# Kernel tuning notes

Measured on AMD Instinct MI355X. Metric: run time of the kernel, lower is better.

Reference implementation:

```python
import jax, jax.numpy as jnp
import numpy as np

L, E, N, D, A = 3, 1000000, 100000, 64, 8
NREL = 230
NR2 = 2 * NREL + 1  # 461 relation embeddings
Q, ENT = 1000, 10000


def setup_inputs() -> dict:
    key = jax.random.key(0)
    ks = jax.random.split(key, 21)
    p = lambda k, shape: jax.random.normal(k, shape, dtype=jnp.float32) * 0.1
    return {
        "relation": jax.random.randint(ks[0], (Q,), 0, NR2, dtype=jnp.int32),
        "r_idx": jax.random.randint(ks[1], (L, E), 0, Q, dtype=jnp.int32),
        "rel": jax.random.randint(ks[2], (L, E), 0, NR2, dtype=jnp.int32),
        "sub": jax.random.randint(ks[3], (L, E), 0, N, dtype=jnp.int32),
        "obj": jax.random.randint(ks[4], (L, E), 0, N, dtype=jnp.int32),
        "idx": jnp.arange(N, dtype=jnp.int32),
        "nodes_q": jax.random.randint(ks[5], (N,), 0, Q, dtype=jnp.int32),
        "nodes_ent": jax.random.randint(ks[6], (N,), 0, ENT, dtype=jnp.int32),
        "rela_embed": p(ks[7], (L, NR2, D)),
        "Ws_w": p(ks[8], (L, A, D)),
        "Wr_w": p(ks[9], (L, A, D)),
        "Wqr_w": p(ks[10], (L, A, D)),
        "Wqr_b": p(ks[11], (L, A)),
        "walpha_w": p(ks[12], (L, 1, A)),
        "walpha_b": p(ks[13], (L, 1)),
        "Wh_w": p(ks[14], (L, D, D)),
        "gru_Wih": p(ks[15], (3 * D, D)),
        "gru_Whh": p(ks[16], (3 * D, D)),
        "gru_bih": p(ks[17], (3 * D,)),
        "gru_bhh": p(ks[18], (3 * D,)),
        "Wfinal_w": p(ks[19], (1, D)),
    }


def _gru_cell(x, h, Wih, Whh, bih, bhh):
    # torch nn.GRU single step: gates from input x and state h
    gi = x @ Wih.T + bih  # [N, 3D]
    gh = h @ Whh.T + bhh  # [N, 3D]
    i_r, i_z, i_n = jnp.split(gi, 3, axis=-1)
    h_r, h_z, h_n = jnp.split(gh, 3, axis=-1)
    r = jax.nn.sigmoid(i_r + h_r)
    z = jax.nn.sigmoid(i_z + h_z)
    n = jnp.tanh(i_n + r * h_n)
    return (1.0 - z) * n + z * h


def reference(relation, r_idx, rel, sub, obj, idx, nodes_q, nodes_ent,
              rela_embed, Ws_w, Wr_w, Wqr_w, Wqr_b, walpha_w, walpha_b, Wh_w,
              gru_Wih, gru_Whh, gru_bih, gru_bhh, Wfinal_w):
    hidden = jnp.zeros((N, D), dtype=jnp.float32)
    h0 = jnp.zeros((N, D), dtype=jnp.float32)
    for i in range(L):  # small fixed number of structurally distinct layers
        emb = rela_embed[i]
        hs = hidden[sub[i]]              # [E, D] gather of source node states
        hr = emb[rel[i]]                 # [E, D] relation embedding lookup
        h_qr = emb[relation[r_idx[i]]]   # [E, D] query-relation embedding
        attn = jax.nn.relu(hs @ Ws_w[i].T + hr @ Wr_w[i].T + h_qr @ Wqr_w[i].T + Wqr_b[i])
        alpha = jax.nn.sigmoid(attn @ walpha_w[i].T + walpha_b[i])  # [E, 1]
        message = alpha * (hs + hr)
        agg = jax.ops.segment_sum(message, obj[i], num_segments=N)  # scatter-add
        hidden = jax.nn.relu(agg @ Wh_w[i].T)
        # index_copy of previous state into new node ordering
        h0 = jnp.zeros((N, D), dtype=jnp.float32).at[idx].set(h0)
        h0 = _gru_cell(hidden, h0, gru_Wih, gru_Whh, gru_bih, gru_bhh)
        hidden = h0
    scores = (hidden @ Wfinal_w.T)[:, 0]  # [N]
    scores_all = jnp.zeros((Q, ENT), dtype=jnp.float32).at[nodes_q, nodes_ent].set(scores)
    return scores_all
```

## Files before the change

### kernel.cpp

```cpp
#include <hip/hip_runtime.h>
#include <math.h>

#define LL  3
#define EE  1000000
#define NNODE 100000
#define DD  64
#define AAT 8
#define NR2C 461
#define QQ  1000
#define ENTC 10000
#define QE  (QQ * ENTC)

#define NB    782
#define NWGL  128
#define CHUNK 7813
#define CAPB  4096

#define SCAN_N (NB * NWGL)
#define SCAN_TILE 4096
#define SCAN_TILES ((SCAN_N + SCAN_TILE - 1) / SCAN_TILE)

#define NTILES (NNODE / 16)
#define NWTILES 58
#define FRAG_U4_PER_LAYER (NWTILES * 2 * 64)

typedef __attribute__((ext_vector_type(8))) short s8v;
typedef __attribute__((ext_vector_type(4))) float f4v;

__device__ __forceinline__ float sigmoidf_(float x) {
    return 1.0f / (1.0f + __expf(-x));
}
__device__ __forceinline__ float tanhf_(float x) {
    return 1.0f - 2.0f / (__expf(2.0f * x) + 1.0f);
}
__device__ __forceinline__ unsigned short bf16rne(float f) {
    unsigned u = __float_as_uint(f);
    return (unsigned short)((u + 0x7FFFu + ((u >> 16) & 1u)) >> 16);
}
__device__ __forceinline__ float bf16tof(unsigned short b) {
    return __uint_as_float(((unsigned)b) << 16);
}

__device__ __forceinline__ float dot8_reduce(float* p, int lane) {
#pragma unroll
    for (int st = 1; st < 8; st <<= 1)
#pragma unroll
        for (int a = 0; a < 8; ++a)
            p[a] += __shfl_xor(p[a], st, 64);
    const int aid = lane & 7;
    float v = p[0];
#pragma unroll
    for (int j = 1; j < 8; ++j)
        v = (aid == j) ? p[j] : v;
    v += __shfl_xor(v, 8, 64);
    v += __shfl_xor(v, 16, 64);
    v += __shfl_xor(v, 32, 64);
    return v;
}

__global__ void fill_f32(float* __restrict__ p, int n, float v) {
    int i = blockIdx.x * blockDim.x + threadIdx.x;
    int stride = gridDim.x * blockDim.x;
    float4* p4 = (float4*)p;
    int n4 = n >> 2;
    float4 v4 = make_float4(v, v, v, v);
    for (int j = i; j < n4; j += stride) p4[j] = v4;
}

__global__ void fill_i32(int* __restrict__ p, int n, int v) {
    int i = blockIdx.x * blockDim.x + threadIdx.x;
    int stride = gridDim.x * blockDim.x;
    int4* p4 = (int4*)p;
    int n4 = n >> 2;
    int4 v4 = make_int4(v, v, v, v);
    for (int j = i; j < n4; j += stride) p4[j] = v4;
}


__global__ __launch_bounds__(256) void part_hist(
    const int* __restrict__ obj, int* __restrict__ hist)
{
    const int l = blockIdx.y, wg = blockIdx.x;
    const int* o = obj + l * EE;
    __shared__ int cnt[NB];
    for (int b = threadIdx.x; b < NB; b += 256) cnt[b] = 0;
    __syncthreads();
    const int s = wg * CHUNK;
    const int e = (s + CHUNK < EE) ? s + CHUNK : EE;
    for (int p = s + threadIdx.x; p < e; p += 256)
        atomicAdd(&cnt[o[p] >> 7], 1);
    __syncthreads();
    int* hh = hist + l * (NB * NWGL);
    for (int b = threadIdx.x; b < NB; b += 256)
        hh[b * NWGL + wg] = cnt[b];
}

__global__ __launch_bounds__(1024) void scan_tiles_reduce(
    const int* __restrict__ hist, int* __restrict__ totals)
{
    const int l = blockIdx.y, tile = blockIdx.x;
    const int* hh = hist + l * SCAN_N;
    const int idx = tile * SCAN_TILE + threadIdx.x * 4;
    int s = 0;
    if (idx < SCAN_N) {
        const int4 v = *(const int4*)(hh + idx);
        s = v.x + v.y + v.z + v.w;
    }
#pragma unroll
    for (int st = 1; st < 64; st <<= 1) s += __shfl_xor(s, st, 64);
    __shared__ int ws[16];
    if ((threadIdx.x & 63) == 0) ws[threadIdx.x >> 6] = s;
    __syncthreads();
    if (threadIdx.x == 0) {
        int t = 0;
#pragma unroll
        for (int i = 0; i < 16; ++i) t += ws[i];
        totals[l * SCAN_TILES + tile] = t;
    }
}

__global__ __launch_bounds__(1024) void scan_tiles_scan(
    int* __restrict__ hist, const int* __restrict__ totals,
    int* __restrict__ bucketptr)
{
    const int l = blockIdx.y, tile = blockIdx.x;
    int* hh = hist + l * SCAN_N;
    int* bp = bucketptr + l * (NB + 1);
    const int t = threadIdx.x;
    __shared__ int lds[1024];
    __shared__ int toff_s;
    if (t < 64) {
        int o = (t < tile) ? totals[l * SCAN_TILES + t] : 0;
#pragma unroll
        for (int st = 1; st < 64; st <<= 1) o += __shfl_xor(o, st, 64);
        if (t == 0) toff_s = o;
    }
    const int idx = tile * SCAN_TILE + t * 4;
    int4 v = make_int4(0, 0, 0, 0);
    if (idx < SCAN_N) v = *(const int4*)(hh + idx);
    const int tsum = v.x + v.y + v.z + v.w;
    lds[t] = tsum;
    __syncthreads();
    for (int st = 1; st < 1024; st <<= 1) {
        const int u = (t >= st) ? lds[t - st] : 0;
        __syncthreads();
        lds[t] += u;
        __syncthreads();
    }
    const int excl = lds[t] - tsum + toff_s;
    if (idx < SCAN_N) {
        int4 o;
        o.x = excl;
        o.y = excl + v.x;
        o.z = o.y + v.y;
        o.w = o.z + v.z;
        *(int4*)(hh + idx) = o;
        if ((idx & 127) == 0) bp[idx >> 7] = o.x;
    }
    if (t == 0 && tile == 0) bp[NB] = EE;
}

__global__ __launch_bounds__(256) void part_scatter(
    const int* __restrict__ obj, const int* __restrict__ sub,
    const int* __restrict__ rel, const int* __restrict__ r_idx,
    const int* __restrict__ hist, unsigned long long* __restrict__ pk64)
{
    const int l = blockIdx.y, wg = blockIdx.x;
    const int* o  = obj + l * EE;
    const int* ss = sub + l * EE;
    const int* rr = rel + l * EE;
    const int* qq = r_idx + l * EE;
    unsigned long long* pk = pk64 + (size_t)l * EE;
    const int* hh = hist + l * (NB * NWGL);
    __shared__ int off[NB];
    for (int b = threadIdx.x; b < NB; b += 256) off[b] = hh[b * NWGL + wg];
    __syncthreads();
    const int s0 = wg * CHUNK;
    const int e0 = (s0 + CHUNK < EE) ? s0 + CHUNK : EE;
    for (int p = s0 + threadIdx.x; p < e0; p += 256) {
        const int ov = o[p];
        const int pos = atomicAdd(&off[ov >> 7], 1);
        pk[pos] = (unsigned long long)(unsigned)ss[p]
                | ((unsigned long long)(unsigned)rr[p] << 17)
                | ((unsigned long long)(unsigned)qq[p] << 26)
                | ((unsigned long long)(unsigned)(ov & 127) << 36);
    }
}

__global__ __launch_bounds__(256) void bucket_sort(
    const int* __restrict__ bucketptr, unsigned long long* __restrict__ pk64,
    int* __restrict__ rowptr)
{
    const int l = blockIdx.y, b = blockIdx.x;
    unsigned long long* pk = pk64 + (size_t)l * EE;
    const int* bp = bucketptr + l * (NB + 1);
    const int base = bp[b], endp = bp[b + 1];
    const int ne = endp - base;
    extern __shared__ unsigned long long stg[];
    __shared__ int cnt[128];
    __shared__ int off[128];
    const int t = threadIdx.x;
    if (t < 128) cnt[t] = 0;
    __syncthreads();
    for (int i = t; i < ne; i += 256) {
        const unsigned long long u = pk[base + i];
        stg[i] = u;
        atomicAdd(&cnt[(int)((u >> 36) & 127)], 1);
    }
    __syncthreads();
    if (t == 0) {
        int run = 0;
#pragma unroll 8
        for (int o2 = 0; o2 < 128; ++o2) { off[o2] = run; run += cnt[o2]; }
    }
    __syncthreads();
    if (t < 128) {
        const int node = b * 128 + t;
        if (node < NNODE) rowptr[l * NNODE + node] = base + off[t] + cnt[t];
    }
    __syncthreads();
    for (int i = t; i < ne; i += 256) {
        const unsigned long long u = stg[i];
        const int pos = base + atomicAdd(&off[(int)((u >> 36) & 127)], 1);
        pk[pos] = u;
    }
}


__global__ __launch_bounds__(256) void rqatt_kernel(
    const int* __restrict__ relation, const float* __restrict__ emb,
    const float* __restrict__ Wr, const float* __restrict__ Wqr,
    const float* __restrict__ Wqrb,
    float* __restrict__ r_att, float* __restrict__ qr_att)
{
    const int lane = threadIdx.x & 63;
    const int wid = (blockIdx.x * blockDim.x + threadIdx.x) >> 6;
    const int nw = (gridDim.x * blockDim.x) >> 6;
    float wr8[8], wq8[8];
#pragma unroll
    for (int a = 0; a < 8; ++a) {
        wr8[a] = Wr[a * 64 + lane];
        wq8[a] = Wqr[a * 64 + lane];
    }
    for (int i = wid; i < NR2C + QQ; i += nw) {
        const bool isQ = i >= NR2C;
        const int row = isQ ? relation[i - NR2C] : i;
        const float ev = emb[row * 64 + lane];
        float p[8];
#pragma unroll
        for (int a = 0; a < 8; ++a) p[a] = ev * (isQ ? wq8[a] : wr8[a]);
        float v = dot8_reduce(p, lane);
        if (lane < 8) {
            if (isQ) qr_att[(i - NR2C) * 8 + lane] = v + Wqrb[lane];
            else     r_att[i * 8 + lane] = v;
        }
    }
}

template<bool L0>
__global__ __launch_bounds__(256) void alpha_csr(
    const unsigned long long* __restrict__ pk64,
    const float* __restrict__ s_att, const float* __restrict__ r_att,
    const float* __restrict__ qr_att,
    const float* __restrict__ walw, const float* __restrict__ walb,
    float* __restrict__ alpha_p)
{
    const int e = blockIdx.x * blockDim.x + threadIdx.x;
    if (e >= EE) return;
    const unsigned long long u = pk64[e];
    const int s = (int)(u & 0x1FFFF);
    const int r = (int)((u >> 17) & 0x1FF);
    const int q = (int)((u >> 26) & 0x3FF);
    const float4* ra = (const float4*)(r_att + r * 8);
    const float4* qa = (const float4*)(qr_att + q * 8);
    const float4 r0 = ra[0], r1 = ra[1];
    const float4 q0 = qa[0], q1 = qa[1];
    float v0 = r0.x + q0.x, v1 = r0.y + q0.y, v2 = r0.z + q0.z, v3 = r0.w + q0.w;
    float v4 = r1.x + q1.x, v5 = r1.y + q1.y, v6 = r1.z + q1.z, v7 = r1.w + q1.w;
    if (!L0) {
        const float4* sa = (const float4*)(s_att + s * 8);
        const float4 s0 = sa[0], s1 = sa[1];
        v0 += s0.x; v1 += s0.y; v2 += s0.z; v3 += s0.w;
        v4 += s1.x; v5 += s1.y; v6 += s1.z; v7 += s1.w;
    }
    float t = walb[0];
    t += walw[0] * fmaxf(v0, 0.0f);
    t += walw[1] * fmaxf(v1, 0.0f);
    t += walw[2] * fmaxf(v2, 0.0f);
    t += walw[3] * fmaxf(v3, 0.0f);
    t += walw[4] * fmaxf(v4, 0.0f);
    t += walw[5] * fmaxf(v5, 0.0f);
    t += walw[6] * fmaxf(v6, 0.0f);
    t += walw[7] * fmaxf(v7, 0.0f);
    alpha_p[e] = sigmoidf_(t);
}

template<bool L0>
__device__ __forceinline__ float gather_term(
    const unsigned long long* __restrict__ pk64,
    const float* __restrict__ alpha_p, int p,
    const float* __restrict__ h, const float* __restrict__ emb, int lane)
{
    const unsigned long long u = pk64[p];
    const float a = alpha_p[p];
    const int s = (int)(u & 0x1FFFF);
    const int r = (int)((u >> 17) & 0x1FF);
    float m = emb[r * 64 + lane];
    if (!L0) m += h[s * 64 + lane];
    return a * m;
}

template<bool L0>
__global__ __launch_bounds__(256) void agg_gather(
    const int* __restrict__ rowptr, const unsigned long long* __restrict__ pk64,
    const float* __restrict__ alpha_p,
    const float* __restrict__ h, const float* __restrict__ emb,
    float* __restrict__ agg)
{
    const int lane = threadIdx.x & 63;
    const int wid = (blockIdx.x * blockDim.x + threadIdx.x) >> 6;
    const int nw = (gridDim.x * blockDim.x) >> 6;
    for (int n = wid; n < NNODE; n += nw) {
        const int start = __builtin_amdgcn_readfirstlane((n == 0) ? 0 : rowptr[n - 1]);
        const int end   = __builtin_amdgcn_readfirstlane(rowptr[n]);
        float a0 = 0.0f, a1 = 0.0f, a2 = 0.0f, a3 = 0.0f;
        int p = start;
        for (; p + 3 < end; p += 4) {
            a0 += gather_term<L0>(pk64, alpha_p, p,     h, emb, lane);
            a1 += gather_term<L0>(pk64, alpha_p, p + 1, h, emb, lane);
            a2 += gather_term<L0>(pk64, alpha_p, p + 2, h, emb, lane);
            a3 += gather_term<L0>(pk64, alpha_p, p + 3, h, emb, lane);
        }
        for (; p < end; ++p)
            a0 += gather_term<L0>(pk64, alpha_p, p, h, emb, lane);
        agg[n * 64 + lane] = (a0 + a1) + (a2 + a3);
    }
}


__global__ __launch_bounds__(128) void build_frags(
    const float* __restrict__ Wh_all, const float* __restrict__ Wih,
    const float* __restrict__ Whh, const float* __restrict__ Ws_all,
    uint4* __restrict__ frag)
{
    const int li = blockIdx.y;
    const int tile = blockIdx.x;
    const int term = threadIdx.x >> 6;
    const int lane_s = threadIdx.x & 63;
    const int rs = lane_s & 15, gs = lane_s >> 4;
    const float* Wh = Wh_all + li * DD * DD;
    const float* WsNext = Ws_all + (li + 1) * AAT * DD;
    unsigned short pk[8];
#pragma unroll
    for (int i = 0; i < 8; ++i) {
        const int kl = 16 * (i >> 2) + 4 * gs + (i & 3);
        float f;
        if (tile < 8)       { const int mt = tile >> 1, kf = tile & 1;
                              f = Wh[(mt * 16 + rs) * 64 + kf * 32 + kl]; }
        else if (tile < 40) { const int t2 = tile - 8, mt = t2 >> 2, kf = t2 & 3;
                              const int j = mt * 16 + rs, k = kf * 32 + kl;
                              f = (k < 64) ? Wih[j * 64 + k] : Whh[j * 64 + k - 64]; }
        else if (tile < 48) { const int t2 = tile - 40, mt = t2 >> 1, kf = t2 & 1;
                              f = Wih[(128 + mt * 16 + rs) * 64 + kf * 32 + kl]; }
        else if (tile < 56) { const int t2 = tile - 48, mt = t2 >> 1, kf = t2 & 1;
                              f = Whh[(128 + mt * 16 + rs) * 64 + kf * 32 + kl]; }
        else                { const int kf = tile - 56;
                              f = (li < 2 && rs < 8) ? WsNext[rs * 64 + kf * 32 + kl] : 0.0f; }
        if (term == 0) pk[i] = bf16rne(f);
        else { const float hi = bf16tof(bf16rne(f)); pk[i] = bf16rne(f - hi); }
    }
    uint4 w;
    w.x = (unsigned)pk[0] | ((unsigned)pk[1] << 16);
    w.y = (unsigned)pk[2] | ((unsigned)pk[3] << 16);
    w.z = (unsigned)pk[4] | ((unsigned)pk[5] << 16);
    w.w = (unsigned)pk[6] | ((unsigned)pk[7] << 16);
    frag[((size_t)li * NWTILES + tile) * 128 + term * 64 + lane_s] = w;
}

__device__ __forceinline__ void make_bfrag(const float* d16, s8v* hi, s8v* lo) {
#pragma unroll
    for (int t = 0; t < 2; ++t) {
        s8v hv, lv;
#pragma unroll
        for (int i = 0; i < 8; ++i) {
            const float f = d16[(2 * t + (i >> 2)) * 4 + (i & 3)];
            const unsigned short hb = bf16rne(f);
            hv[i] = (short)hb;
            lv[i] = (short)bf16rne(f - bf16tof(hb));
        }
        hi[t] = hv; lo[t] = lv;
    }
}

__device__ __forceinline__ f4v mm3(const s8v* __restrict__ afr, int tile, int lane,
                                   s8v bh, s8v bl, f4v c) {
    const s8v ah = afr[(tile * 2 + 0) * 64 + lane];
    const s8v al = afr[(tile * 2 + 1) * 64 + lane];
    c = __builtin_amdgcn_mfma_f32_16x16x32_bf16(ah, bh, c, 0, 0, 0);
    c = __builtin_amdgcn_mfma_f32_16x16x32_bf16(ah, bl, c, 0, 0, 0);
    c = __builtin_amdgcn_mfma_f32_16x16x32_bf16(al, bh, c, 0, 0, 0);
    return c;
}

__device__ __forceinline__ void ld16(const float* p, float* d) {
#pragma unroll
    for (int mt = 0; mt < 4; ++mt) {
        const float4 v = *(const float4*)(p + 16 * mt);
        d[mt * 4 + 0] = v.x; d[mt * 4 + 1] = v.y;
        d[mt * 4 + 2] = v.z; d[mt * 4 + 3] = v.w;
    }
}

template<bool L0, bool SATT, bool SCORE>
__global__ __launch_bounds__(256, 4) void node_mfma(
    const uint4* __restrict__ frag,
    const float* __restrict__ bih, const float* __restrict__ bhh,
    const float* __restrict__ Wf,
    float* __restrict__ h, const float* __restrict__ agg,
    float* __restrict__ s_att, float* __restrict__ scores)
{
    const int tid = threadIdx.x;
    const int lane = tid & 63;
    const int wslot = (blockIdx.x * 256 + tid) >> 6;
    const int base = wslot * 16;
    if (base >= NNODE) return;
    const int r = lane & 15, g = lane >> 4;
    const s8v* afr = (const s8v*)frag;

    float ag[16], hp[16];
    ld16(agg + (base + r) * 64 + 4 * g, ag);
    if (!L0) ld16(h + (base + r) * 64 + 4 * g, hp);
    else {
#pragma unroll
        for (int i = 0; i < 16; ++i) hp[i] = 0.0f;
    }
    s8v agh[2], agl[2];
    make_bfrag(ag, agh, agl);
    s8v hh2[2], hl2[2];
    if (!L0) make_bfrag(hp, hh2, hl2);

    float xd[16];
#pragma unroll
    for (int mt = 0; mt < 4; ++mt) {
        f4v acc = {0.0f, 0.0f, 0.0f, 0.0f};
        acc = mm3(afr, mt * 2 + 0, lane, agh[0], agl[0], acc);
        acc = mm3(afr, mt * 2 + 1, lane, agh[1], agl[1], acc);
#pragma unroll
        for (int c = 0; c < 4; ++c) xd[mt * 4 + c] = fmaxf(acc[c], 0.0f);
    }
    s8v xh[2], xl[2];
    make_bfrag(xd, xh, xl);

    f4v rz[8];
#pragma unroll
    for (int mt = 0; mt < 4; ++mt) {
        const int j0 = 16 * mt + 4 * g;
        const float4 a = *(const float4*)(bih + j0);
        const float4 b = *(const float4*)(bhh + j0);
        f4v t; t[0] = a.x + b.x; t[1] = a.y + b.y; t[2] = a.z + b.z; t[3] = a.w + b.w;
        rz[mt] = t;
        const float4 a2 = *(const float4*)(bih + 64 + j0);
        const float4 b2 = *(const float4*)(bhh + 64 + j0);
        f4v t2; t2[0] = a2.x + b2.x; t2[1] = a2.y + b2.y; t2[2] = a2.z + b2.z; t2[3] = a2.w + b2.w;
        rz[mt + 4] = t2;
    }
#pragma unroll
    for (int mt = 0; mt < 8; ++mt) {
        f4v acc = rz[mt];
        acc = mm3(afr, 8 + mt * 4 + 0, lane, xh[0], xl[0], acc);
        acc = mm3(afr, 8 + mt * 4 + 1, lane, xh[1], xl[1], acc);
        if (!L0) {
            acc = mm3(afr, 8 + mt * 4 + 2, lane, hh2[0], hl2[0], acc);
            acc = mm3(afr, 8 + mt * 4 + 3, lane, hh2[1], hl2[1], acc);
        }
        rz[mt] = acc;
    }

    f4v in4[4], hn4[4];
#pragma unroll
    for (int mt = 0; mt < 4; ++mt) {
        const int j0 = 16 * mt + 4 * g;
        const float4 a = *(const float4*)(bih + 128 + j0);
        f4v t; t[0] = a.x; t[1] = a.y; t[2] = a.z; t[3] = a.w;
        in4[mt] = t;
        const float4 b = *(const float4*)(bhh + 128 + j0);
        f4v t2; t2[0] = b.x; t2[1] = b.y; t2[2] = b.z; t2[3] = b.w;
        hn4[mt] = t2;
    }
#pragma unroll
    for (int mt = 0; mt < 4; ++mt) {
        f4v acc = in4[mt];
        acc = mm3(afr, 40 + mt * 2 + 0, lane, xh[0], xl[0], acc);
        acc = mm3(afr, 40 + mt * 2 + 1, lane, xh[1], xl[1], acc);
        in4[mt] = acc;
        if (!L0) {
            f4v a2 = hn4[mt];
            a2 = mm3(afr, 48 + mt * 2 + 0, lane, hh2[0], hl2[0], a2);
            a2 = mm3(afr, 48 + mt * 2 + 1, lane, hh2[1], hl2[1], a2);
            hn4[mt] = a2;
        }
    }

    float ho[16];
#pragma unroll
    for (int mt = 0; mt < 4; ++mt)
#pragma unroll
        for (int c = 0; c < 4; ++c) {
            const float rr = sigmoidf_(rz[mt][c]);
            const float zz = sigmoidf_(rz[mt + 4][c]);
            const float nn = tanhf_(in4[mt][c] + rr * hn4[mt][c]);
            ho[mt * 4 + c] = (1.0f - zz) * nn + zz * hp[mt * 4 + c];
        }

    if (!SCORE) {
        float* hop = h + (base + r) * 64 + 4 * g;
#pragma unroll
        for (int mt = 0; mt < 4; ++mt)
            *(float4*)(hop + 16 * mt) = make_float4(ho[mt * 4 + 0], ho[mt * 4 + 1],
                                                    ho[mt * 4 + 2], ho[mt * 4 + 3]);
    }
    if (SATT) {
        s8v oh[2], ol[2];
        make_bfrag(ho, oh, ol);
        f4v sa = {0.0f, 0.0f, 0.0f, 0.0f};
        sa = mm3(afr, 56, lane, oh[0], ol[0], sa);
        sa = mm3(afr, 57, lane, oh[1], ol[1], sa);
        if (g < 2) {
#pragma unroll
            for (int c = 0; c < 4; ++c)
                s_att[(base + r) * 8 + 4 * g + c] = sa[c];
        }
    }
    if (SCORE) {
        float s = 0.0f;
        const float* wfp = Wf + 4 * g;
#pragma unroll
        for (int mt = 0; mt < 4; ++mt) {
            const float4 w = *(const float4*)(wfp + 16 * mt);
            s += ho[mt * 4 + 0] * w.x + ho[mt * 4 + 1] * w.y
               + ho[mt * 4 + 2] * w.z + ho[mt * 4 + 3] * w.w;
        }
        s += __shfl_xor(s, 16, 64);
        s += __shfl_xor(s, 32, 64);
        if (lane < 16) scores[base + r] = s;
    }
}

__global__ void scatter_max_kernel(const int* __restrict__ nq, const int* __restrict__ ne,
                                   int* __restrict__ winner)
{
    int n = blockIdx.x * blockDim.x + threadIdx.x;
    if (n < NNODE) {
        int pos = nq[n] * ENTC + ne[n];
        atomicMax(&winner[pos], n);
    }
}

__global__ void scatter_write_kernel(const int* __restrict__ nq, const int* __restrict__ ne,
                                     const int* __restrict__ winner,
                                     const float* __restrict__ scores,
                                     float* __restrict__ out)
{
    int n = blockIdx.x * blockDim.x + threadIdx.x;
    if (n < NNODE) {
        int pos = nq[n] * ENTC + ne[n];
        if (winner[pos] == n) out[pos] = scores[n];
    }
}

extern "C" void kernel_launch(void* const* d_in, const int* in_sizes, int n_in,
                              void* d_out, int out_size, void* d_ws, size_t ws_size,
                              hipStream_t stream)
{
    const int* relation  = (const int*)d_in[0];
    const int* r_idx     = (const int*)d_in[1];
    const int* rel       = (const int*)d_in[2];
    const int* sub       = (const int*)d_in[3];
    const int* obj       = (const int*)d_in[4];
    const int* nodes_q   = (const int*)d_in[6];
    const int* nodes_ent = (const int*)d_in[7];
    const float* rela    = (const float*)d_in[8];
    const float* Ws      = (const float*)d_in[9];
    const float* Wr      = (const float*)d_in[10];
    const float* Wqr     = (const float*)d_in[11];
    const float* Wqrb    = (const float*)d_in[12];
    const float* walw    = (const float*)d_in[13];
    const float* walb    = (const float*)d_in[14];
    const float* Wh      = (const float*)d_in[15];
    const float* gWih    = (const float*)d_in[16];
    const float* gWhh    = (const float*)d_in[17];
    const float* gbih    = (const float*)d_in[18];
    const float* gbhh    = (const float*)d_in[19];
    const float* Wf      = (const float*)d_in[20];

    float* ws     = (float*)d_ws;
    float* scores = ws;
    float* h      = ws + 102400;
    float* agg    = h + NNODE * DD;
    int*   winner = (int*)(ws + 102400);
    float* out    = (float*)d_out;

    unsigned long long* pk64 = (unsigned long long*)d_out;
    uint4* fragbuf  = (uint4*)((float*)d_out + 6000000);
    float* s_att    = (float*)d_out + 6000000 + 3 * FRAG_U4_PER_LAYER * 4;
    float* r_att    = s_att + NNODE * 8;
    float* qr_att   = r_att + NR2C * 8;
    int*   rowptr   = (int*)(qr_att + QQ * 8);
    int*   hist     = rowptr + 3 * NNODE;
    int*   bucketpt = hist + 3 * NB * NWGL;
    int*   totals   = bucketpt + 3 * (NB + 1);
    float* alpha_p  = (float*)(totals + 3 * SCAN_TILES);

    part_hist<<<dim3(NWGL, 3), 256, 0, stream>>>(obj, hist);
    scan_tiles_reduce<<<dim3(SCAN_TILES, 3), 1024, 0, stream>>>(hist, totals);
    scan_tiles_scan<<<dim3(SCAN_TILES, 3), 1024, 0, stream>>>(hist, totals, bucketpt);
    part_scatter<<<dim3(NWGL, 3), 256, 0, stream>>>(obj, sub, rel, r_idx, hist, pk64);
    bucket_sort<<<dim3(NB, 3), 256, CAPB * 8, stream>>>(bucketpt, pk64, rowptr);
    build_frags<<<dim3(NWTILES, 3), 128, 0, stream>>>(Wh, gWih, gWhh, Ws, fragbuf);

    const int NODE_GRID = (NTILES * 64 + 255) / 256;
    for (int i = 0; i < LL; ++i) {
        const float* emb = rela + i * NR2C * DD;
        const uint4* fr = fragbuf + (size_t)i * FRAG_U4_PER_LAYER;
        rqatt_kernel<<<184, 256, 0, stream>>>(relation, emb,
            Wr + i * AAT * DD, Wqr + i * AAT * DD, Wqrb + i * AAT, r_att, qr_att);
        if (i == 0) {
            alpha_csr<true><<<(EE + 255) / 256, 256, 0, stream>>>(
                pk64, s_att, r_att, qr_att, walw, walb, alpha_p);
            agg_gather<true><<<2048, 256, 0, stream>>>(
                rowptr, pk64, alpha_p, h, emb, agg);
            node_mfma<true, true, false><<<NODE_GRID, 256, 0, stream>>>(
                fr, gbih, gbhh, Wf, h, agg, s_att, scores);
        } else {
            alpha_csr<false><<<(EE + 255) / 256, 256, 0, stream>>>(
                pk64 + (size_t)i * EE, s_att, r_att, qr_att,
                walw + i * AAT, walb + i, alpha_p);
            agg_gather<false><<<2048, 256, 0, stream>>>(
                rowptr + i * NNODE, pk64 + (size_t)i * EE, alpha_p, h, emb, agg);
            if (i == 1)
                node_mfma<false, true, false><<<NODE_GRID, 256, 0, stream>>>(
                    fr, gbih, gbhh, Wf, h, agg, s_att, scores);
            else
                node_mfma<false, false, true><<<NODE_GRID, 256, 0, stream>>>(
                    fr, gbih, gbhh, Wf, h, agg, s_att, scores);
        }
    }

    fill_f32<<<2048, 256, 0, stream>>>(out, QE, 0.0f);
    fill_i32<<<2048, 256, 0, stream>>>(winner, QE, -1);
    scatter_max_kernel<<<(NNODE + 255) / 256, 256, 0, stream>>>(nodes_q, nodes_ent, winner);
    scatter_write_kernel<<<(NNODE + 255) / 256, 256, 0, stream>>>(nodes_q, nodes_ent, winner, scores, out);
}
```

Measured before the change: 601.8 us.

## Stage partition scatter and bucket sort in LDS for coalesced global writes

```diff
diff --git a/kernel.cpp b/kernel.cpp
--- a/kernel.cpp
+++ b/kernel.cpp
@@ -16,6 +16,8 @@
 #define CHUNK 7813
 #define CAPB  4096
 
+#define PS_LDS (CHUNK * 8 + NB * 4 * 2 + 256 * 4)
+
 #define SCAN_N (NB * NWGL)
 #define SCAN_TILE 4096
 #define SCAN_TILES ((SCAN_N + SCAN_TILE - 1) / SCAN_TILE)
@@ -165,6 +167,10 @@
     const int* __restrict__ rel, const int* __restrict__ r_idx,
     const int* __restrict__ hist, unsigned long long* __restrict__ pk64)
 {
+    extern __shared__ unsigned long long stg[];
+    int* cnt   = (int*)(stg + CHUNK);
+    int* delta = cnt + NB;
+    int* psum  = delta + NB;
     const int l = blockIdx.y, wg = blockIdx.x;
     const int* o  = obj + l * EE;
     const int* ss = sub + l * EE;
@@ -172,18 +178,64 @@
     const int* qq = r_idx + l * EE;
     unsigned long long* pk = pk64 + (size_t)l * EE;
     const int* hh = hist + l * (NB * NWGL);
-    __shared__ int off[NB];
-    for (int b = threadIdx.x; b < NB; b += 256) off[b] = hh[b * NWGL + wg];
-    __syncthreads();
+    const int t = threadIdx.x;
     const int s0 = wg * CHUNK;
     const int e0 = (s0 + CHUNK < EE) ? s0 + CHUNK : EE;
-    for (int p = s0 + threadIdx.x; p < e0; p += 256) {
+    const int ne = e0 - s0;
+
+    for (int b = t; b < NB; b += 256) cnt[b] = 0;
+    __syncthreads();
+    for (int p = s0 + t; p < e0; p += 256)
+        atomicAdd(&cnt[o[p] >> 7], 1);
+    __syncthreads();
+
+    {
+        const int b0 = t * 4;
+        int local[4];
+        int s = 0;
+#pragma unroll
+        for (int j = 0; j < 4; ++j) {
+            const int idx = b0 + j;
+            local[j] = (idx < NB) ? cnt[idx] : 0;
+            s += local[j];
+        }
+        psum[t] = s;
+        __syncthreads();
+        for (int st = 1; st < 256; st <<= 1) {
+            const int v = (t >= st) ? psum[t - st] : 0;
+            __syncthreads();
+            psum[t] += v;
+            __syncthreads();
+        }
+        int run = (t == 0) ? 0 : psum[t - 1];
+#pragma unroll
+        for (int j = 0; j < 4; ++j) {
+            const int idx = b0 + j;
+            if (idx < NB) {
+                cnt[idx] = run;
+                delta[idx] = hh[idx * NWGL + wg] - run;
+                run += local[j];
+            }
+        }
+    }
+    __syncthreads();
+
+    for (int p = s0 + t; p < e0; p += 256) {
         const int ov = o[p];
-        const int pos = atomicAdd(&off[ov >> 7], 1);
-        pk[pos] = (unsigned long long)(unsigned)ss[p]
-                | ((unsigned long long)(unsigned)rr[p] << 17)
-                | ((unsigned long long)(unsigned)qq[p] << 26)
-                | ((unsigned long long)(unsigned)(ov & 127) << 36);
+        const int b = ov >> 7;
+        const int k = atomicAdd(&cnt[b], 1);
+        stg[k] = (unsigned long long)(unsigned)ss[p]
+               | ((unsigned long long)(unsigned)rr[p] << 17)
+               | ((unsigned long long)(unsigned)qq[p] << 26)
+               | ((unsigned long long)(unsigned)(ov & 127) << 36)
+               | ((unsigned long long)(unsigned)b << 43);
+    }
+    __syncthreads();
+
+    for (int i = t; i < ne; i += 256) {
+        const unsigned long long u = stg[i];
+        const int b = (int)((u >> 43) & 0x3FF);
+        pk[delta[b] + i] = u;
     }
 }
 
@@ -197,6 +249,7 @@
     const int base = bp[b], endp = bp[b + 1];
     const int ne = endp - base;
     extern __shared__ unsigned long long stg[];
+    unsigned long long* srt = stg + CAPB;
     __shared__ int cnt[128];
     __shared__ int off[128];
     const int t = threadIdx.x;
@@ -221,9 +274,12 @@
     __syncthreads();
     for (int i = t; i < ne; i += 256) {
         const unsigned long long u = stg[i];
-        const int pos = base + atomicAdd(&off[(int)((u >> 36) & 127)], 1);
-        pk[pos] = u;
-    }
+        const int pos = atomicAdd(&off[(int)((u >> 36) & 127)], 1);
+        srt[pos] = u;
+    }
+    __syncthreads();
+    for (int i = t; i < ne; i += 256)
+        pk[base + i] = srt[i];
 }
 
 
@@ -614,8 +670,8 @@
     part_hist<<<dim3(NWGL, 3), 256, 0, stream>>>(obj, hist);
     scan_tiles_reduce<<<dim3(SCAN_TILES, 3), 1024, 0, stream>>>(hist, totals);
     scan_tiles_scan<<<dim3(SCAN_TILES, 3), 1024, 0, stream>>>(hist, totals, bucketpt);
-    part_scatter<<<dim3(NWGL, 3), 256, 0, stream>>>(obj, sub, rel, r_idx, hist, pk64);
-    bucket_sort<<<dim3(NB, 3), 256, CAPB * 8, stream>>>(bucketpt, pk64, rowptr);
+    part_scatter<<<dim3(NWGL, 3), 256, PS_LDS, stream>>>(obj, sub, rel, r_idx, hist, pk64);
+    bucket_sort<<<dim3(NB, 3), 256, CAPB * 16, stream>>>(bucketpt, pk64, rowptr);
     build_frags<<<dim3(NWTILES, 3), 128, 0, stream>>>(Wh, gWih, gWhh, Ws, fragbuf);
 
     const int NODE_GRID = (NTILES * 64 + 255) / 256;
```

After: 579.9 us. -3.6%, faster.
